# Kernel tuning notes

Measured on AMD Instinct MI355X. Metric: run time of the kernel, lower is better.

## Reference

```python
import jax, jax.numpy as jnp
import numpy as np

D_MODEL = 1024
N_HEADS = 16
D_KV = D_MODEL // N_HEADS
MAX_SEQ = 2048
THETA = 10000.0
BATCH = 2
SEQ = 2048


def setup_inputs() -> dict:
    key = jax.random.key(0)
    ks = jax.random.split(key, 5)
    std = np.sqrt(2.0 / (D_MODEL + D_MODEL))
    x = jax.random.normal(ks[0], (BATCH, SEQ, D_MODEL), dtype=jnp.float32)
    wq = jax.random.normal(ks[1], (D_MODEL, D_MODEL), dtype=jnp.float32) * std
    wk = jax.random.normal(ks[2], (D_MODEL, D_MODEL), dtype=jnp.float32) * std
    wv = jax.random.normal(ks[3], (D_MODEL, D_MODEL), dtype=jnp.float32) * std
    wo = jax.random.normal(ks[4], (D_MODEL, D_MODEL), dtype=jnp.float32) * std
    token_positions = jnp.arange(SEQ, dtype=jnp.int32)
    return {"x": x, "wq": wq, "wk": wk, "wv": wv, "wo": wo,
            "token_positions": token_positions}


def _rope_tables():
    freq_range = jnp.arange(D_KV // 2, dtype=jnp.float32)
    freq = 1.0 / (THETA ** (2.0 * freq_range / D_KV))
    pos = jnp.arange(MAX_SEQ, dtype=jnp.float32)
    angs = pos[:, None] * freq[None, :]  # [max_seq, d_kv/2]
    return jnp.cos(angs), jnp.sin(angs)


def _apply_rope(xh, token_positions, cos_t, sin_t):
    # xh: [b, h, s, d_kv]
    cos_f = jnp.repeat(cos_t[token_positions], 2, axis=-1)  # [s, d_kv]
    sin_f = jnp.repeat(sin_t[token_positions], 2, axis=-1)
    pairs = xh.reshape(*xh.shape[:-1], D_KV // 2, 2)
    even, odd = pairs[..., 0], pairs[..., 1]
    rot = jnp.stack([-odd, even], axis=-1).reshape(xh.shape)
    return xh * cos_f + rot * sin_f


def reference(x, wq, wk, wv, wo, token_positions):
    b, s, _ = x.shape
    def heads(y):
        return y.reshape(b, s, N_HEADS, D_KV).transpose(0, 2, 1, 3)  # [b,h,s,d]
    q = heads(jnp.einsum('bsi,oi->bso', x, wq))
    k = heads(jnp.einsum('bsi,oi->bso', x, wk))
    v = heads(jnp.einsum('bsi,oi->bso', x, wv))
    cos_t, sin_t = _rope_tables()
    q = _apply_rope(q, token_positions, cos_t, sin_t)
    k = _apply_rope(k, token_positions, cos_t, sin_t)
    scale = 1.0 / jnp.sqrt(jnp.asarray(D_KV, x.dtype))
    scores = jnp.einsum('bhqd,bhkd->bhqk', q, k) * scale
    causal = jnp.tril(jnp.ones((s, s), dtype=bool))
    scores = jnp.where(causal, scores, -jnp.inf)
    probs = jax.nn.softmax(scores, axis=-1)
    attn = jnp.einsum('bhqk,bhkd->bhqd', probs, v)
    attn = attn.transpose(0, 2, 1, 3).reshape(b, s, D_MODEL)
    return jnp.einsum('bsi,oi->bso', attn, wo)
```

## Files before the change

### kernel.cpp

```cpp
#include <hip/hip_runtime.h>
#include <hip/hip_bf16.h>
#include <math.h>

#define SEQ 2048
#define DM 1024
#define NH 16
#define DKV 64
#define MTOT 4096
#define PST2 72

typedef __attribute__((ext_vector_type(8))) short bf16x8;
typedef __attribute__((ext_vector_type(4))) short s16x4;
typedef __attribute__((ext_vector_type(4))) float f32x4;
typedef unsigned short ushort_t;

__device__ __forceinline__ short f2bf(float f) {
    union { float f; unsigned u; } v; v.f = f;
    unsigned r = v.u + 0x7fffu + ((v.u >> 16) & 1u);
    return (short)(r >> 16);
}

__device__ __forceinline__ bf16x8 cvt8(f32x4 a, f32x4 b) {
    union { __hip_bfloat162 h[4]; bf16x8 v; } u;
    u.h[0] = __float22bfloat162_rn(float2{a[0], a[1]});
    u.h[1] = __float22bfloat162_rn(float2{a[2], a[3]});
    u.h[2] = __float22bfloat162_rn(float2{b[0], b[1]});
    u.h[3] = __float22bfloat162_rn(float2{b[2], b[3]});
    return u.v;
}

__device__ __forceinline__ s16x4 cvt4(float a, float b, float c, float d) {
    union { __hip_bfloat162 h[2]; s16x4 v; } u;
    u.h[0] = __float22bfloat162_rn(float2{a, b});
    u.h[1] = __float22bfloat162_rn(float2{c, d});
    return u.v;
}

__device__ __forceinline__ void gload_lds16(const void* g, void* l) {
    __builtin_amdgcn_global_load_lds(
        (const __attribute__((address_space(1))) unsigned int*)g,
        (__attribute__((address_space(3))) unsigned int*)l, 16, 0, 0);
}

__global__ void prep_kernel(const float* __restrict__ x,
                            const float* __restrict__ wq, const float* __restrict__ wk,
                            const float* __restrict__ wv, const float* __restrict__ wo,
                            ushort_t* __restrict__ Wqkv, ushort_t* __restrict__ xb,
                            ushort_t* __restrict__ Wob,
                            float* __restrict__ cos_t, float* __restrict__ sin_t) {
    const int b = blockIdx.x;
    if (b < 256) {
        int tid = b * 256 + threadIdx.x;
        int i = tid & 31, pos = tid >> 5;
        float freq = expf(-9.210340372f * (float)(2 * i) / 64.0f);
        float ang = (float)pos * freq;
        cos_t[tid] = cosf(ang);
        sin_t[tid] = sinf(ang);
    } else if (b < 768) {
        int tid = (b - 256) * 256 + threadIdx.x;
        int off = tid * 8;
        f32x4 a = ((const f32x4*)(wo + off))[0];
        f32x4 c = ((const f32x4*)(wo + off))[1];
        *(bf16x8*)&Wob[off] = cvt8(a, c);
    } else if (b < 2304) {
        int tid = (b - 768) * 256 + threadIdx.x;
        int z = tid >> 17;
        int off = (tid & 131071) * 8;
        const float* src = (z == 0) ? wq : (z == 1) ? wk : wv;
        f32x4 a = ((const f32x4*)(src + off))[0];
        f32x4 c = ((const f32x4*)(src + off))[1];
        *(bf16x8*)&Wqkv[(size_t)z * 1048576 + off] = cvt8(a, c);
    } else {
        int tid = (b - 2304) * 256 + threadIdx.x;
        int off = tid * 8;
        f32x4 a = ((const f32x4*)(x + off))[0];
        f32x4 c = ((const f32x4*)(x + off))[1];
        *(bf16x8*)&xb[off] = cvt8(a, c);
    }
}

__global__ __launch_bounds__(256) void proj_qkv_kernel(
    const ushort_t* __restrict__ xb, const ushort_t* __restrict__ Wqkv,
    const float* __restrict__ cos_t, const float* __restrict__ sin_t,
    const int* __restrict__ tokpos,
    ushort_t* __restrict__ Qg, ushort_t* __restrict__ Kg, ushort_t* __restrict__ Vt)
{
    __shared__ __align__(16) short lA[3][128 * 32];
    __shared__ __align__(16) short lB[3][64 * 32];

    const int t = threadIdx.x;
    const int lane = t & 63;
    const int wid = t >> 6;
    const int quad = lane >> 4, l16 = lane & 15;
    const int mh = wid >> 1, nh = wid & 1;
    const int Mb = blockIdx.y * 128;
    const int NbG = blockIdx.x * 64;
    const int z = NbG >> 10;
    const int Nb = NbG & 1023;

    f32x4 acc[4][2] = {};

    auto stage = [&](int buf, int k0) {
        #pragma unroll
        for (int i = 0; i < 2; ++i) {
            int rbase = wid * 32 + i * 16;
            int row = rbase + (lane >> 2);
            int gch = (lane & 3) ^ ((lane >> 3) & 3);
            gload_lds16(xb + (size_t)(Mb + row) * DM + k0 + gch * 8, &lA[buf][rbase * 32]);
        }
        {
            int rbase = wid * 16;
            int row = rbase + (lane >> 2);
            int gch = (lane & 3) ^ ((lane >> 3) & 3);
            gload_lds16(Wqkv + (size_t)(NbG + row) * DM + k0 + gch * 8, &lB[buf][rbase * 32]);
        }
    };

    stage(0, 0);
    stage(1, 32);

    for (int kt = 0; kt < 32; ++kt) {
        const int cur = kt % 3;
        if (kt == 31) asm volatile("s_waitcnt vmcnt(0)" ::: "memory");
        else          asm volatile("s_waitcnt vmcnt(3)" ::: "memory");
        __builtin_amdgcn_s_barrier();
        if (kt < 30) stage((kt + 2) % 3, kt * 32 + 64);

        bf16x8 a[4], b[2];
        #pragma unroll
        for (int mt = 0; mt < 4; ++mt) {
            int row = mh * 64 + mt * 16 + l16;
            int slot = quad ^ ((l16 >> 1) & 3);
            a[mt] = *(const bf16x8*)&lA[cur][row * 32 + slot * 8];
        }
        #pragma unroll
        for (int nt = 0; nt < 2; ++nt) {
            int row = nh * 32 + nt * 16 + l16;
            int slot = quad ^ ((l16 >> 1) & 3);
            b[nt] = *(const bf16x8*)&lB[cur][row * 32 + slot * 8];
        }
        __builtin_amdgcn_s_setprio(1);
        #pragma unroll
        for (int mt = 0; mt < 4; ++mt)
            #pragma unroll
            for (int nt = 0; nt < 2; ++nt)
                acc[mt][nt] = __builtin_amdgcn_mfma_f32_16x16x32_bf16(a[mt], b[nt], acc[mt][nt], 0, 0, 0);
        __builtin_amdgcn_s_setprio(0);
    }

    const int bb = Mb >> 11;
    if (z == 2) {
        #pragma unroll
        for (int mt = 0; mt < 4; ++mt) {
            const int s0 = (Mb + mh * 64 + mt * 16 + quad * 4) & (SEQ - 1);
            #pragma unroll
            for (int nt = 0; nt < 2; ++nt) {
                int col = Nb + nh * 32 + nt * 16 + l16;
                int h = col >> 6, d = col & 63;
                s16x4 pk;
                #pragma unroll
                for (int r = 0; r < 4; ++r) pk[r] = f2bf(acc[mt][nt][r]);
                *(s16x4*)&Vt[((size_t)(bb * NH + h) * DKV + d) * SEQ + s0] = pk;
            }
        }
    } else {
        ushort_t* dst = (z == 0) ? Qg : Kg;
        const float qscale = (z == 0) ? 0.125f : 1.0f;
        #pragma unroll
        for (int mt = 0; mt < 4; ++mt) {
            #pragma unroll
            for (int nt = 0; nt < 2; ++nt) {
                #pragma unroll
                for (int r = 0; r < 4; ++r) {
                    int row = Mb + mh * 64 + mt * 16 + quad * 4 + r;
                    int s = row & (SEQ - 1);
                    int col = Nb + nh * 32 + nt * 16 + l16;
                    int h = col >> 6, d = col & 63;
                    float val = acc[mt][nt][r];
                    float part = __shfl_xor(val, 1, 64);
                    int pos = tokpos[s];
                    int i = d >> 1;
                    float c = cos_t[pos * 32 + i];
                    float sn = sin_t[pos * 32 + i];
                    val = (d & 1) ? (val * c + part * sn) : (val * c - part * sn);
                    val *= qscale;
                    dst[((size_t)(bb * NH + h) * SEQ + s) * DKV + d] = (ushort_t)f2bf(val);
                }
            }
        }
    }
}

__global__ __launch_bounds__(256, 2) void attn_kernel(
    const ushort_t* __restrict__ Q, const ushort_t* __restrict__ K,
    const ushort_t* __restrict__ Vt, ushort_t* __restrict__ O)
{
    __shared__ __align__(16) short lK[2][2][64 * 64];
    __shared__ __align__(16) short lV[2][2][64 * 64];
    __shared__ __align__(16) short lP[4][16 * PST2];

    const int t = threadIdx.x;
    const int lane = t & 63;
    const int wid = t >> 6;
    const int quad = lane >> 4, l16 = lane & 15;
    const int bh = blockIdx.y;
    const int bb = bh >> 4, h = bh & 15;

    const ushort_t* Qb = Q + (size_t)bh * SEQ * DKV;
    const ushort_t* Kb = K + (size_t)bh * SEQ * DKV;
    const ushort_t* Vtb = Vt + (size_t)bh * DKV * SEQ;
    short* myP = lP[wid];

    auto stage = [&](int kb, int buf) {
        #pragma unroll
        for (int hf = 0; hf < 2; ++hf) {
            #pragma unroll
            for (int j = 0; j < 2; ++j) {
                int rbase = wid * 16 + j * 8;
                int row = rbase + (lane >> 3);
                int gch = (lane & 7) ^ (row & 7);
                gload_lds16(Kb + (size_t)(kb + hf * 64 + row) * DKV + gch * 8,
                            &lK[buf][hf][rbase * 64]);
            }
            #pragma unroll
            for (int j = 0; j < 2; ++j) {
                int rbase = wid * 16 + j * 8;
                int row = rbase + (lane >> 3);
                int gch = (lane & 7) ^ (row & 7);
                gload_lds16(Vtb + (size_t)row * SEQ + kb + hf * 64 + gch * 8,
                            &lV[buf][hf][rbase * 64]);
            }
        }
    };

    #pragma unroll 1
    for (int ph = 0; ph < 2; ++ph) {
        const int qt = ph ? (31 - (int)blockIdx.x) : (int)blockIdx.x;
        const int q0w = qt * 64 + wid * 16;
        const int nkt2 = (qt >> 1) + 1;

        bf16x8 bq[2];
        #pragma unroll
        for (int hq = 0; hq < 2; ++hq)
            bq[hq] = *(const bf16x8*)(Qb + (size_t)(q0w + l16) * DKV + hq * 32 + quad * 8);

        f32x4 acc[4] = {};
        float ps = 0.f;

        if (ph) __syncthreads();
        stage(0, 0);

        for (int kt2 = 0; kt2 < nkt2; ++kt2) {
            const int kb128 = kt2 * 128;
            __syncthreads();
            if (kt2 + 1 < nkt2) stage(kb128 + 128, (kt2 + 1) & 1);

            #pragma unroll
            for (int hf = 0; hf < 2; ++hf) {
                const int kbase = kb128 + hf * 64;
                if (kbase > q0w + 15) continue;

                const short* bK = lK[kt2 & 1][hf];
                const short* bV = lV[kt2 & 1][hf];

                bf16x8 ak[4][2];
                #pragma unroll
                for (int mt = 0; mt < 4; ++mt)
                    #pragma unroll
                    for (int hh = 0; hh < 2; ++hh) {
                        int row = mt * 16 + l16;
                        int slot = (hh * 4 + quad) ^ (row & 7);
                        ak[mt][hh] = *(const bf16x8*)&bK[row * 64 + slot * 8];
                    }

                f32x4 st[4];
                __builtin_amdgcn_s_setprio(1);
                #pragma unroll
                for (int mt = 0; mt < 4; ++mt) {
                    f32x4 zz = {};
                    zz = __builtin_amdgcn_mfma_f32_16x16x32_bf16(ak[mt][0], bq[0], zz, 0, 0, 0);
                    zz = __builtin_amdgcn_mfma_f32_16x16x32_bf16(ak[mt][1], bq[1], zz, 0, 0, 0);
                    st[mt] = zz;
                }
                __builtin_amdgcn_s_setprio(0);

                if (kbase + 63 > q0w) {
                    #pragma unroll
                    for (int mt = 0; mt < 4; ++mt) {
                        float pv[4];
                        #pragma unroll
                        for (int r = 0; r < 4; ++r) {
                            int k_abs = kbase + mt * 16 + quad * 4 + r;
                            int q_abs = q0w + l16;
                            pv[r] = (k_abs > q_abs) ? 0.f : __expf(st[mt][r]);
                            ps += pv[r];
                        }
                        *(s16x4*)&myP[l16 * PST2 + mt * 16 + quad * 4] = cvt4(pv[0], pv[1], pv[2], pv[3]);
                    }
                } else {
                    #pragma unroll
                    for (int mt = 0; mt < 4; ++mt) {
                        float pv[4];
                        #pragma unroll
                        for (int r = 0; r < 4; ++r) {
                            pv[r] = __expf(st[mt][r]);
                            ps += pv[r];
                        }
                        *(s16x4*)&myP[l16 * PST2 + mt * 16 + quad * 4] = cvt4(pv[0], pv[1], pv[2], pv[3]);
                    }
                }

                bf16x8 ap[2];
                ap[0] = *(const bf16x8*)&myP[l16 * PST2 + quad * 8];
                ap[1] = *(const bf16x8*)&myP[l16 * PST2 + 32 + quad * 8];

                __builtin_amdgcn_s_setprio(1);
                #pragma unroll
                for (int d = 0; d < 4; ++d) {
                    int row = d * 16 + l16;
                    int slot0 = quad ^ (row & 7);
                    int slot1 = (4 + quad) ^ (row & 7);
                    bf16x8 bv0 = *(const bf16x8*)&bV[row * 64 + slot0 * 8];
                    bf16x8 bv1 = *(const bf16x8*)&bV[row * 64 + slot1 * 8];
                    acc[d] = __builtin_amdgcn_mfma_f32_16x16x32_bf16(ap[0], bv0, acc[d], 0, 0, 0);
                    acc[d] = __builtin_amdgcn_mfma_f32_16x16x32_bf16(ap[1], bv1, acc[d], 0, 0, 0);
                }
                __builtin_amdgcn_s_setprio(0);
            }
        }

        ps += __shfl_xor(ps, 16, 64);
        ps += __shfl_xor(ps, 32, 64);
        float* lLw = (float*)myP;
        if (quad == 0) lLw[l16] = ps;
        f32x4 lv = *(const f32x4*)&lLw[quad * 4];
        f32x4 inv;
        #pragma unroll
        for (int r = 0; r < 4; ++r) inv[r] = 1.0f / lv[r];
        #pragma unroll
        for (int d = 0; d < 4; ++d)
            #pragma unroll
            for (int r = 0; r < 4; ++r) {
                int qrow = q0w + quad * 4 + r;
                int dd = d * 16 + l16;
                O[(size_t)(bb * SEQ + qrow) * DM + h * DKV + dd] = (ushort_t)f2bf(acc[d][r] * inv[r]);
            }
    }
}

__global__ __launch_bounds__(256) void oproj_kernel(
    const ushort_t* __restrict__ A, const ushort_t* __restrict__ B, float* __restrict__ out)
{
    __shared__ __align__(16) short lA[3][128 * 32];
    __shared__ __align__(16) short lB[3][64 * 32];

    const int t = threadIdx.x;
    const int lane = t & 63;
    const int wid = t >> 6;
    const int quad = lane >> 4, l16 = lane & 15;
    const int mh = wid >> 1, nh = wid & 1;
    const int Mb = blockIdx.y * 128;
    const int Nb = blockIdx.x * 64;

    f32x4 acc[4][2] = {};

    auto stage = [&](int buf, int k0) {
        #pragma unroll
        for (int i = 0; i < 2; ++i) {
            int rbase = wid * 32 + i * 16;
            int row = rbase + (lane >> 2);
            int gch = (lane & 3) ^ ((lane >> 3) & 3);
            gload_lds16(A + (size_t)(Mb + row) * DM + k0 + gch * 8, &lA[buf][rbase * 32]);
        }
        {
            int rbase = wid * 16;
            int row = rbase + (lane >> 2);
            int gch = (lane & 3) ^ ((lane >> 3) & 3);
            gload_lds16(B + (size_t)(Nb + row) * DM + k0 + gch * 8, &lB[buf][rbase * 32]);
        }
    };

    stage(0, 0);
    stage(1, 32);

    for (int kt = 0; kt < 32; ++kt) {
        const int cur = kt % 3;
        if (kt == 31) asm volatile("s_waitcnt vmcnt(0)" ::: "memory");
        else          asm volatile("s_waitcnt vmcnt(3)" ::: "memory");
        __builtin_amdgcn_s_barrier();
        if (kt < 30) stage((kt + 2) % 3, kt * 32 + 64);

        bf16x8 a[4], b[2];
        #pragma unroll
        for (int mt = 0; mt < 4; ++mt) {
            int row = mh * 64 + mt * 16 + l16;
            int slot = quad ^ ((l16 >> 1) & 3);
            a[mt] = *(const bf16x8*)&lA[cur][row * 32 + slot * 8];
        }
        #pragma unroll
        for (int nt = 0; nt < 2; ++nt) {
            int row = nh * 32 + nt * 16 + l16;
            int slot = quad ^ ((l16 >> 1) & 3);
            b[nt] = *(const bf16x8*)&lB[cur][row * 32 + slot * 8];
        }
        __builtin_amdgcn_s_setprio(1);
        #pragma unroll
        for (int mt = 0; mt < 4; ++mt)
            #pragma unroll
            for (int nt = 0; nt < 2; ++nt)
                acc[mt][nt] = __builtin_amdgcn_mfma_f32_16x16x32_bf16(a[mt], b[nt], acc[mt][nt], 0, 0, 0);
        __builtin_amdgcn_s_setprio(0);
    }

    #pragma unroll
    for (int mt = 0; mt < 4; ++mt)
        #pragma unroll
        for (int nt = 0; nt < 2; ++nt)
            #pragma unroll
            for (int r = 0; r < 4; ++r) {
                int row = Mb + mh * 64 + mt * 16 + quad * 4 + r;
                int col = Nb + nh * 32 + nt * 16 + l16;
                out[(size_t)row * DM + col] = acc[mt][nt][r];
            }
}

extern "C" void kernel_launch(void* const* d_in, const int* in_sizes, int n_in,
                              void* d_out, int out_size, void* d_ws, size_t ws_size,
                              hipStream_t stream) {
    const float* x  = (const float*)d_in[0];
    const float* wq = (const float*)d_in[1];
    const float* wk = (const float*)d_in[2];
    const float* wv = (const float*)d_in[3];
    const float* wo = (const float*)d_in[4];
    const int* tokpos = (const int*)d_in[5];
    float* out = (float*)d_out;

    char* ws = (char*)d_ws;
    float* cos_t    = (float*)ws;
    float* sin_t    = (float*)(ws + 256 * 1024);
    ushort_t* Wqkv  = (ushort_t*)(ws + 512 * 1024);
    ushort_t* AO    = (ushort_t*)ws;
    ushort_t* Qg    = (ushort_t*)(ws + (size_t)8  * 1024 * 1024);
    ushort_t* Kg    = (ushort_t*)(ws + (size_t)16 * 1024 * 1024);
    ushort_t* Wob   = (ushort_t*)(ws + (size_t)24 * 1024 * 1024);
    ushort_t* xb    = (ushort_t*)d_out;
    ushort_t* Vt    = (ushort_t*)((char*)d_out + (size_t)8 * 1024 * 1024);

    prep_kernel<<<4352, 256, 0, stream>>>(x, wq, wk, wv, wo, Wqkv, xb, Wob, cos_t, sin_t);
    proj_qkv_kernel<<<dim3(3 * DM / 64, MTOT / 128), 256, 0, stream>>>(
        xb, Wqkv, cos_t, sin_t, tokpos, Qg, Kg, Vt);
    attn_kernel<<<dim3(SEQ / 128, 32), 256, 0, stream>>>(Qg, Kg, Vt, AO);
    oproj_kernel<<<dim3(DM / 64, MTOT / 128), 256, 0, stream>>>(AO, Wob, out);
}
```

Baseline: 203.2 us.

## Enlarge QKV projection tiles to 256x256 with 8 waves and BK=64

The QKV projection GEMM now uses 256x256 output tiles per block with 512 threads (8 waves, each owning a 128x64 sub-tile). K steps are 64 wide with an 8-way XOR swizzle, and the triple-buffered pipeline becomes a double buffer. The goal is more reuse of each loaded operand and fewer global loads per MFMA. In exchange the grid shrinks to 192 blocks, fewer than the CU count, and there is a full vmcnt(0) wait every iteration plus 128 KB of LDS and high accumulator register pressure.

```diff
diff --git a/kernel.cpp b/kernel.cpp
--- a/kernel.cpp
+++ b/kernel.cpp
@@ -79,87 +79,90 @@
     }
 }
 
-__global__ __launch_bounds__(256) void proj_qkv_kernel(
+__global__ __launch_bounds__(512) void proj_qkv_kernel(
     const ushort_t* __restrict__ xb, const ushort_t* __restrict__ Wqkv,
     const float* __restrict__ cos_t, const float* __restrict__ sin_t,
     const int* __restrict__ tokpos,
     ushort_t* __restrict__ Qg, ushort_t* __restrict__ Kg, ushort_t* __restrict__ Vt)
 {
-    __shared__ __align__(16) short lA[3][128 * 32];
-    __shared__ __align__(16) short lB[3][64 * 32];
+    __shared__ __align__(16) short lA[2][256 * 64];
+    __shared__ __align__(16) short lB[2][256 * 64];
 
     const int t = threadIdx.x;
     const int lane = t & 63;
     const int wid = t >> 6;
     const int quad = lane >> 4, l16 = lane & 15;
-    const int mh = wid >> 1, nh = wid & 1;
-    const int Mb = blockIdx.y * 128;
-    const int NbG = blockIdx.x * 64;
+    const int wm = wid >> 2, wn = wid & 3;
+    const int Mb = blockIdx.y * 256;
+    const int NbG = blockIdx.x * 256;
     const int z = NbG >> 10;
     const int Nb = NbG & 1023;
 
-    f32x4 acc[4][2] = {};
-
-    auto stage = [&](int buf, int k0) {
-        #pragma unroll
-        for (int i = 0; i < 2; ++i) {
-            int rbase = wid * 32 + i * 16;
-            int row = rbase + (lane >> 2);
-            int gch = (lane & 3) ^ ((lane >> 3) & 3);
-            gload_lds16(xb + (size_t)(Mb + row) * DM + k0 + gch * 8, &lA[buf][rbase * 32]);
-        }
-        {
-            int rbase = wid * 16;
-            int row = rbase + (lane >> 2);
-            int gch = (lane & 3) ^ ((lane >> 3) & 3);
-            gload_lds16(Wqkv + (size_t)(NbG + row) * DM + k0 + gch * 8, &lB[buf][rbase * 32]);
+    f32x4 acc[8][4] = {};
+
+    auto stage = [&](int kt, int buf) {
+        const int k0 = kt * 64;
+        #pragma unroll
+        for (int j = 0; j < 4; ++j) {
+            int rbase = wid * 32 + j * 8;
+            int row = rbase + (lane >> 3);
+            int gch = (lane & 7) ^ (row & 7);
+            gload_lds16(xb + (size_t)(Mb + row) * DM + k0 + gch * 8, &lA[buf][rbase * 64]);
+        }
+        #pragma unroll
+        for (int j = 0; j < 4; ++j) {
+            int rbase = wid * 32 + j * 8;
+            int row = rbase + (lane >> 3);
+            int gch = (lane & 7) ^ (row & 7);
+            gload_lds16(Wqkv + (size_t)(NbG + row) * DM + k0 + gch * 8, &lB[buf][rbase * 64]);
         }
     };
 
     stage(0, 0);
-    stage(1, 32);
-
-    for (int kt = 0; kt < 32; ++kt) {
-        const int cur = kt % 3;
-        if (kt == 31) asm volatile("s_waitcnt vmcnt(0)" ::: "memory");
-        else          asm volatile("s_waitcnt vmcnt(3)" ::: "memory");
+
+    for (int kt = 0; kt < 16; ++kt) {
+        const int cur = kt & 1;
+        asm volatile("s_waitcnt vmcnt(0)" ::: "memory");
         __builtin_amdgcn_s_barrier();
-        if (kt < 30) stage((kt + 2) % 3, kt * 32 + 64);
-
-        bf16x8 a[4], b[2];
-        #pragma unroll
-        for (int mt = 0; mt < 4; ++mt) {
-            int row = mh * 64 + mt * 16 + l16;
-            int slot = quad ^ ((l16 >> 1) & 3);
-            a[mt] = *(const bf16x8*)&lA[cur][row * 32 + slot * 8];
-        }
-        #pragma unroll
-        for (int nt = 0; nt < 2; ++nt) {
-            int row = nh * 32 + nt * 16 + l16;
-            int slot = quad ^ ((l16 >> 1) & 3);
-            b[nt] = *(const bf16x8*)&lB[cur][row * 32 + slot * 8];
-        }
-        __builtin_amdgcn_s_setprio(1);
-        #pragma unroll
-        for (int mt = 0; mt < 4; ++mt)
-            #pragma unroll
-            for (int nt = 0; nt < 2; ++nt)
-                acc[mt][nt] = __builtin_amdgcn_mfma_f32_16x16x32_bf16(a[mt], b[nt], acc[mt][nt], 0, 0, 0);
-        __builtin_amdgcn_s_setprio(0);
+        if (kt < 15) stage(kt + 1, cur ^ 1);
+
+        #pragma unroll
+        for (int ks = 0; ks < 2; ++ks) {
+            bf16x8 a[8], b[4];
+            #pragma unroll
+            for (int mf = 0; mf < 8; ++mf) {
+                int row = wm * 128 + mf * 16 + l16;
+                int slot = (ks * 4 + quad) ^ (row & 7);
+                a[mf] = *(const bf16x8*)&lA[cur][row * 64 + slot * 8];
+            }
+            #pragma unroll
+            for (int nf = 0; nf < 4; ++nf) {
+                int row = wn * 64 + nf * 16 + l16;
+                int slot = (ks * 4 + quad) ^ (row & 7);
+                b[nf] = *(const bf16x8*)&lB[cur][row * 64 + slot * 8];
+            }
+            __builtin_amdgcn_s_setprio(1);
+            #pragma unroll
+            for (int mf = 0; mf < 8; ++mf)
+                #pragma unroll
+                for (int nf = 0; nf < 4; ++nf)
+                    acc[mf][nf] = __builtin_amdgcn_mfma_f32_16x16x32_bf16(a[mf], b[nf], acc[mf][nf], 0, 0, 0);
+            __builtin_amdgcn_s_setprio(0);
+        }
     }
 
     const int bb = Mb >> 11;
     if (z == 2) {
         #pragma unroll
-        for (int mt = 0; mt < 4; ++mt) {
-            const int s0 = (Mb + mh * 64 + mt * 16 + quad * 4) & (SEQ - 1);
-            #pragma unroll
-            for (int nt = 0; nt < 2; ++nt) {
-                int col = Nb + nh * 32 + nt * 16 + l16;
+        for (int mf = 0; mf < 8; ++mf) {
+            const int s0 = (Mb + wm * 128 + mf * 16 + quad * 4) & (SEQ - 1);
+            #pragma unroll
+            for (int nf = 0; nf < 4; ++nf) {
+                int col = Nb + wn * 64 + nf * 16 + l16;
                 int h = col >> 6, d = col & 63;
                 s16x4 pk;
                 #pragma unroll
-                for (int r = 0; r < 4; ++r) pk[r] = f2bf(acc[mt][nt][r]);
+                for (int r = 0; r < 4; ++r) pk[r] = f2bf(acc[mf][nf][r]);
                 *(s16x4*)&Vt[((size_t)(bb * NH + h) * DKV + d) * SEQ + s0] = pk;
             }
         }
@@ -167,16 +170,16 @@
         ushort_t* dst = (z == 0) ? Qg : Kg;
         const float qscale = (z == 0) ? 0.125f : 1.0f;
         #pragma unroll
-        for (int mt = 0; mt < 4; ++mt) {
-            #pragma unroll
-            for (int nt = 0; nt < 2; ++nt) {
+        for (int mf = 0; mf < 8; ++mf) {
+            #pragma unroll
+            for (int nf = 0; nf < 4; ++nf) {
                 #pragma unroll
                 for (int r = 0; r < 4; ++r) {
-                    int row = Mb + mh * 64 + mt * 16 + quad * 4 + r;
+                    int row = Mb + wm * 128 + mf * 16 + quad * 4 + r;
                     int s = row & (SEQ - 1);
-                    int col = Nb + nh * 32 + nt * 16 + l16;
+                    int col = Nb + wn * 64 + nf * 16 + l16;
                     int h = col >> 6, d = col & 63;
-                    float val = acc[mt][nt][r];
+                    float val = acc[mf][nf][r];
                     float part = __shfl_xor(val, 1, 64);
                     int pos = tokpos[s];
                     int i = d >> 1;
@@ -447,7 +450,7 @@
     ushort_t* Vt    = (ushort_t*)((char*)d_out + (size_t)8 * 1024 * 1024);
 
     prep_kernel<<<4352, 256, 0, stream>>>(x, wq, wk, wv, wo, Wqkv, xb, Wob, cos_t, sin_t);
-    proj_qkv_kernel<<<dim3(3 * DM / 64, MTOT / 128), 256, 0, stream>>>(
+    proj_qkv_kernel<<<dim3(3 * DM / 256, MTOT / 256), 512, 0, stream>>>(
         xb, Wqkv, cos_t, sin_t, tokpos, Qg, Kg, Vt);
     attn_kernel<<<dim3(SEQ / 128, 32), 256, 0, stream>>>(Qg, Kg, Vt, AO);
     oproj_kernel<<<dim3(DM / 64, MTOT / 128), 256, 0, stream>>>(AO, Wob, out);
```

Result: faster. 193.2 us (median of 2 runs) (-4.9%).
